# Kernel optimization log

Measured on AMD Instinct MI355X. Metric: run time of the kernel, lower is better.

## Reference

```python
import jax, jax.numpy as jnp
import numpy as np

DEPTH = 5
EPS = 1e-8


def setup_inputs() -> dict:
    key = jax.random.key(0)
    ks = jax.random.split(key, 7)
    N, E, Q = 50000, 1600000, 16
    return {
        "marg_i": jax.random.normal(ks[0], (N, Q), dtype=jnp.float32),
        "cav_ij": jax.random.uniform(ks[1], (E, Q), dtype=jnp.float32),
        "C": jax.random.uniform(ks[2], (Q, Q), dtype=jnp.float32),
        "field_i": jax.random.normal(ks[3], (N, Q), dtype=jnp.float32),
        "edge_dst": jax.random.randint(ks[4], (E,), 0, N, dtype=jnp.int32),
        "a1_src": jax.random.randint(ks[5], (E,), 0, N, dtype=jnp.int32),
        "indice_ij": jax.random.randint(ks[6], (E,), 0, E, dtype=jnp.int32),
    }


def reference(marg_i, cav_ij, C, field_i, edge_dst, a1_src, indice_ij):
    # Belief-propagation layers repeated DEPTH times.
    # B_ @ temp2  -> segment_sum of edge messages into destination nodes [N,Q]
    # A1 @ marg_i -> gather of source-node marginal per edge [E,Q]
    N = field_i.shape[0]

    def step(carry, _):
        marg, cav = carry
        temp2 = jnp.log(cav @ C + EPS)                                  # [E,Q]
        marg = jax.ops.segment_sum(temp2, edge_dst, num_segments=N) + field_i  # [N,Q]
        cav = jax.nn.softmax(marg[a1_src] - temp2[indice_ij], axis=1)  # [E,Q]
        return (marg, cav), None

    (marg, cav), _ = jax.lax.scan(step, (marg_i, cav_ij), None, length=DEPTH)
    return jax.nn.log_softmax(marg, axis=1)
```

## Files before the change

kernel.cpp:

```cpp
#include <hip/hip_runtime.h>
#include <hip/hip_fp16.h>

#define Q 16
#define EPS 1e-8f
#define DEPTH 5

typedef unsigned int u32;
typedef _Float16 h2 __attribute__((ext_vector_type(2)));

__device__ __forceinline__ u32 pack2(float a, float b) {
    __half2 h = __floats2half2_rn(a, b);
    return *(u32*)&h;
}
__device__ __forceinline__ float2 unpack2(u32 u) {
    __half2 h = *(__half2*)&u;
    return __half22float2(h);
}
__device__ __forceinline__ h2 mkh2(float a, float b) {
    h2 v; v[0] = (_Float16)a; v[1] = (_Float16)b; return v;
}


__global__ __launch_bounds__(256) void rank0_kernel(
    const int* __restrict__ dst, int* __restrict__ count,
    int* __restrict__ lr, int E)
{
    int e = blockIdx.x * 256 + threadIdx.x;
    if (e < E) lr[e] = atomicAdd(&count[dst[e]], 1);
}

__global__ __launch_bounds__(256) void scan_partial(
    const int* __restrict__ count, int* __restrict__ partial, int N)
{
    __shared__ int sm[256];
    int i = blockIdx.x * 256 + threadIdx.x;
    sm[threadIdx.x] = (i < N) ? count[i] : 0;
    __syncthreads();
    for (int off = 128; off > 0; off >>= 1) {
        if (threadIdx.x < off) sm[threadIdx.x] += sm[threadIdx.x + off];
        __syncthreads();
    }
    if (threadIdx.x == 0) partial[blockIdx.x] = sm[0];
}

__global__ __launch_bounds__(1024) void scan_top(
    int* __restrict__ partial, int nb)
{
    __shared__ int sm[1024];
    int t = threadIdx.x;
    int v = (t < nb) ? partial[t] : 0;
    sm[t] = v;
    __syncthreads();
    for (int off = 1; off < 1024; off <<= 1) {
        int u = (t >= off) ? sm[t - off] : 0;
        __syncthreads();
        sm[t] += u;
        __syncthreads();
    }
    if (t < nb) partial[t] = sm[t] - v;
}

__global__ __launch_bounds__(256) void scan_final(
    const int* __restrict__ count, const int* __restrict__ partial,
    int* __restrict__ start, int N)
{
    __shared__ int sm[256];
    int i = blockIdx.x * 256 + threadIdx.x;
    int v = (i < N) ? count[i] : 0;
    sm[threadIdx.x] = v;
    __syncthreads();
    for (int off = 1; off < 256; off <<= 1) {
        int u = (threadIdx.x >= off) ? sm[threadIdx.x - off] : 0;
        __syncthreads();
        sm[threadIdx.x] += u;
        __syncthreads();
    }
    int excl = sm[threadIdx.x] - v + partial[blockIdx.x];
    if (i < N) start[i] = excl;
    if (i == N - 1) start[N] = excl + v;
}

__global__ __launch_bounds__(256) void pos_kernel(
    const int* __restrict__ dst, const int* __restrict__ lr,
    const int* __restrict__ start, int* __restrict__ pos, int E)
{
    int e = blockIdx.x * 256 + threadIdx.x;
    if (e < E) pos[e] = start[dst[e]] + lr[e];
}

__global__ __launch_bounds__(256) void scatter_direct(
    const int* __restrict__ a1_src, const int* __restrict__ indice,
    const int* __restrict__ dst, const int* __restrict__ pos,
    int4* __restrict__ sorted, int E)
{
    int e = blockIdx.x * 256 + threadIdx.x;
    if (e < E)
        sorted[pos[e]] = make_int4(a1_src[e], pos[indice[e]], dst[e], e);
}

__global__ __launch_bounds__(256) void meta_pack(
    const int4* __restrict__ sorted, int2* __restrict__ meta2, int E)
{
    int j = blockIdx.x * 256 + threadIdx.x;
    if (j < E) {
        int4 m = sorted[j];
        meta2[j] = make_int2(m.y, (m.z << 16) | m.x);
    }
}

__global__ __launch_bounds__(256) void bnode_build(
    const int* __restrict__ start, int* __restrict__ blist,
    int* __restrict__ bcount, int N)
{
    int n = blockIdx.x * 256 + threadIdx.x;
    if (n >= N) return;
    int slo = start[n], shi = start[n + 1];
    bool need = (slo == shi) || ((slo >> 8) != ((shi - 1) >> 8));
    if (need) {
        int p = atomicAdd(bcount, 1);
        blist[p] = n;
    }
}

__global__ __launch_bounds__(256) void binit(
    const int* __restrict__ blist, const int* __restrict__ bcount,
    const float* __restrict__ field, float* __restrict__ marg)
{
    int idx = blockIdx.x * 256 + threadIdx.x;
    int cnt = *bcount;
    if (idx >= cnt * 4) return;
    int n = blist[idx >> 2], part = idx & 3;
    ((float4*)(marg + (size_t)n * Q))[part] =
        ((const float4*)(field + (size_t)n * Q))[part];
}

template<int MODE>
__global__ __launch_bounds__(256) void fused_round(
    const int4* __restrict__ sorted, const int2* __restrict__ meta2,
    const float* __restrict__ C,
    const float* __restrict__ cav,
    const float* __restrict__ marg_in, const u32* __restrict__ t2_old,
    const int* __restrict__ start, const float* __restrict__ field,
    u32* __restrict__ t2_new, float* __restrict__ marg_out, int E)
{
    __shared__ __align__(16) h2 Csh[Q * 8];
    __shared__ float stage[256 * 17];
    __shared__ int s_nfirst, s_nlast;

    const int tid = threadIdx.x;
    const int blo = blockIdx.x * 256;
    const int bhi = min(blo + 256, E);
    const int j = blo + tid;
    const bool act = (j < E);

    int4 smeta;
    int2 meta;
    float4 m0, m1, m2, m3;
    uint4 r0, r1;
    if (MODE == 0) {
        if (act) {
            smeta = sorted[j];
            const float4* rp = (const float4*)(cav + (size_t)smeta.w * Q);
            m0 = rp[0]; m1 = rp[1]; m2 = rp[2]; m3 = rp[3];
        }
    } else {
        if (act) {
            meta = meta2[j];
            const int src = meta.y & 0xffff;
            const float4* mp = (const float4*)(marg_in + (size_t)src * Q);
            const uint4*  tp = (const uint4*)(t2_old + (size_t)meta.x * 8);
            m0 = mp[0]; m1 = mp[1]; m2 = mp[2]; m3 = mp[3];
            r0 = tp[0]; r1 = tp[1];
        }
    }

    if (tid < 128) {
        int q = tid >> 3, kk = tid & 7;
        Csh[q * 8 + kk] = mkh2(C[(2 * kk) * Q + q], C[(2 * kk + 1) * Q + q]);
    }
    if (act) {
        int mydst = (MODE == 0) ? smeta.z : (int)(((u32)meta.y) >> 16);
        if (j == blo)     s_nfirst = mydst;
        if (j == bhi - 1) s_nlast  = mydst;
    }
    __syncthreads();

    float t[Q];
    if (act) {
        h2 uh[8];
        float s, logs;
        if (MODE == 0) {
            uh[0] = mkh2(m0.x, m0.y); uh[1] = mkh2(m0.z, m0.w);
            uh[2] = mkh2(m1.x, m1.y); uh[3] = mkh2(m1.z, m1.w);
            uh[4] = mkh2(m2.x, m2.y); uh[5] = mkh2(m2.z, m2.w);
            uh[6] = mkh2(m3.x, m3.y); uh[7] = mkh2(m3.z, m3.w);
            s = 1.f; logs = 0.f;
        } else {
            float2 p0 = unpack2(r0.x), p1 = unpack2(r0.y),
                   p2 = unpack2(r0.z), p3 = unpack2(r0.w);
            float2 p4 = unpack2(r1.x), p5 = unpack2(r1.y),
                   p6 = unpack2(r1.z), p7 = unpack2(r1.w);

            float x[Q] = {m0.x - p0.x, m0.y - p0.y, m0.z - p1.x, m0.w - p1.y,
                          m1.x - p2.x, m1.y - p2.y, m1.z - p3.x, m1.w - p3.y,
                          m2.x - p4.x, m2.y - p4.y, m2.z - p5.x, m2.w - p5.y,
                          m3.x - p6.x, m3.y - p6.y, m3.z - p7.x, m3.w - p7.y};

            float mx = x[0];
#pragma unroll
            for (int q = 1; q < Q; ++q) mx = fmaxf(mx, x[q]);
            float u[Q];
            s = 0.f;
#pragma unroll
            for (int q = 0; q < Q; ++q) { u[q] = __expf(x[q] - mx); s += u[q]; }
            logs = __logf(s);
#pragma unroll
            for (int k = 0; k < 8; ++k) uh[k] = mkh2(u[2 * k], u[2 * k + 1]);
        }

        const float base = EPS * s;
#pragma unroll
        for (int q = 0; q < Q; ++q) {
            const uint4* cp = (const uint4*)&Csh[q * 8];
            h2 col[8];
            ((uint4*)col)[0] = cp[0];
            ((uint4*)col)[1] = cp[1];
            float acc = base;
#pragma unroll
            for (int kk = 0; kk < 8; ++kk)
                acc = __builtin_amdgcn_fdot2(uh[kk], col[kk], acc, false);
            t[q] = __logf(acc) - logs;
        }

        if (MODE != 2) {
            uint4 w0, w1;
            w0.x = pack2(t[0],  t[1]);  w0.y = pack2(t[2],  t[3]);
            w0.z = pack2(t[4],  t[5]);  w0.w = pack2(t[6],  t[7]);
            w1.x = pack2(t[8],  t[9]);  w1.y = pack2(t[10], t[11]);
            w1.z = pack2(t[12], t[13]); w1.w = pack2(t[14], t[15]);
            uint4* op = (uint4*)(t2_new + (size_t)j * 8);
            op[0] = w0; op[1] = w1;
        }
    } else {
#pragma unroll
        for (int q = 0; q < Q; ++q) t[q] = 0.f;
    }

#pragma unroll
    for (int q = 0; q < Q; ++q) stage[tid * 17 + q] = t[q];
    __syncthreads();

    const int nfirst = s_nfirst;
    const int ncnt = s_nlast - nfirst + 1;
    for (int k = tid; k < ncnt * Q; k += 256) {
        int ln = k >> 4, q = k & 15;
        int n = nfirst + ln;
        int slo = start[n], shi = start[n + 1];
        int lo = max(slo, blo), hi = min(shi, bhi);
        float s = 0.f;
        for (int sl = lo; sl < hi; ++sl) s += stage[(sl - blo) * 17 + q];
        if (slo >= blo && shi <= bhi)
            marg_out[(size_t)n * Q + q] = s + field[(size_t)n * Q + q];
        else
            atomicAdd(marg_out + (size_t)n * Q + q, s);
    }
}

__global__ __launch_bounds__(256) void node_out(
    const float* __restrict__ marg, float* __restrict__ out, int N)
{
    int i = blockIdx.x * 256 + threadIdx.x;
    if (i >= N) return;

    const float4* mp = (const float4*)(marg + (size_t)i * Q);
    float4 m0 = mp[0], m1 = mp[1], m2 = mp[2], m3 = mp[3];
    float x[Q] = {m0.x, m0.y, m0.z, m0.w, m1.x, m1.y, m1.z, m1.w,
                  m2.x, m2.y, m2.z, m2.w, m3.x, m3.y, m3.z, m3.w};

    float mx = x[0];
#pragma unroll
    for (int q = 1; q < Q; ++q) mx = fmaxf(mx, x[q]);
    float s = 0.f;
#pragma unroll
    for (int q = 0; q < Q; ++q) s += __expf(x[q] - mx);
    float lse = mx + __logf(s);

    float4* op = (float4*)(out + (size_t)i * Q);
    op[0] = make_float4(x[0]  - lse, x[1]  - lse, x[2]  - lse, x[3]  - lse);
    op[1] = make_float4(x[4]  - lse, x[5]  - lse, x[6]  - lse, x[7]  - lse);
    op[2] = make_float4(x[8]  - lse, x[9]  - lse, x[10] - lse, x[11] - lse);
    op[3] = make_float4(x[12] - lse, x[13] - lse, x[14] - lse, x[15] - lse);
}

extern "C" void kernel_launch(void* const* d_in, const int* in_sizes, int n_in,
                              void* d_out, int out_size, void* d_ws, size_t ws_size,
                              hipStream_t stream) {
    const float* cav_in   = (const float*)d_in[1];
    const float* C        = (const float*)d_in[2];
    const float* field_i  = (const float*)d_in[3];
    const int*   edge_dst = (const int*)d_in[4];
    const int*   a1_src   = (const int*)d_in[5];
    const int*   indice   = (const int*)d_in[6];
    float* out = (float*)d_out;

    const int E = in_sizes[4];
    const int N = in_sizes[0] / Q;

    char* ws = (char*)d_ws;
    const size_t t2_bytes   = (size_t)E * 32;
    const size_t i4_bytes   = (size_t)E * 16;
    const size_t node_bytes = (size_t)N * Q * sizeof(float);
    u32*   t2a    = (u32*)ws;                     ws += t2_bytes;
    u32*   t2b    = (u32*)ws;                     ws += t2_bytes;
    int4*  sorted = (int4*)ws;                    ws += i4_bytes;
    int2*  meta2  = (int2*)ws;                    ws += (size_t)E * 8;
    float* marg_a = (float*)ws;                   ws += node_bytes;
    float* marg_b = (float*)ws;                   ws += node_bytes;
    int*   pos    = (int*)ws;                     ws += (size_t)E * 4;
    int*   lr     = (int*)ws;                     ws += (size_t)E * 4;
    int*   count  = (int*)ws;                     ws += (size_t)N * 4;
    int*   bcount = (int*)ws;                     ws += 4;
    int*   start  = (int*)ws;                     ws += (size_t)(N + 1) * 4;
    int*   blist  = (int*)ws;                     ws += (size_t)N * 4;
    int*   partial= (int*)ws;

    const int eb = 256;
    const int eg = (E + eb - 1) / eb;
    const int ng = (N + eb - 1) / eb;

    hipMemsetAsync(count, 0, (size_t)N * 4 + 4, stream);
    rank0_kernel<<<eg, eb, 0, stream>>>(edge_dst, count, lr, E);
    scan_partial<<<ng, eb, 0, stream>>>(count, partial, N);
    scan_top<<<1, 1024, 0, stream>>>(partial, ng);
    scan_final<<<ng, eb, 0, stream>>>(count, partial, start, N);
    pos_kernel<<<eg, eb, 0, stream>>>(edge_dst, lr, start, pos, E);
    scatter_direct<<<eg, eb, 0, stream>>>(a1_src, indice, edge_dst, pos, sorted, E);
    meta_pack<<<eg, eb, 0, stream>>>(sorted, meta2, E);
    bnode_build<<<ng, eb, 0, stream>>>(start, blist, bcount, N);

    u32* t_cur = t2a;
    u32* t_nxt = t2b;
    float* m_in = marg_b;
    float* m_out = marg_a;
    const int bg = (N * 4 + eb - 1) / eb;

    for (int it = 0; it < DEPTH; ++it) {
        binit<<<bg, eb, 0, stream>>>(blist, bcount, field_i, m_out);
        if (it == 0)
            fused_round<0><<<eg, eb, 0, stream>>>(sorted, meta2, C, cav_in,
                                                  nullptr, nullptr, start, field_i,
                                                  t_cur, m_out, E);
        else if (it != DEPTH - 1)
            fused_round<1><<<eg, eb, 0, stream>>>(sorted, meta2, C, nullptr,
                                                  m_in, t_cur, start, field_i,
                                                  t_nxt, m_out, E);
        else
            fused_round<2><<<eg, eb, 0, stream>>>(sorted, meta2, C, nullptr,
                                                  m_in, t_cur, start, field_i,
                                                  nullptr, m_out, E);
        if (it != 0) { u32* tt = t_cur; t_cur = t_nxt; t_nxt = tt; }
        float* tm = m_in; m_in = m_out; m_out = tm;
    }

    node_out<<<ng, eb, 0, stream>>>(m_in, out, N);
}
```

Baseline: 608.0 us.

## Push temp2 to consumer slots via scatter instead of gathering by indice

Builds a CSR of consumers (edges whose indice points at each producer edge) during preprocessing, so each round a producer writes its half-precision temp2 row directly into every consumer's slot. The next round then reads its t2 row contiguously at j instead of gathering at a random sorted index. Metadata is also shrunk from int4/int2 to packed 4-byte arrays. In exchange, preprocessing gains extra atomics, a second multi-level scan and a scatter kernel, and the per-round writes become random scatters whose count varies per edge, which adds divergence.

```diff
diff --git a/kernel.cpp b/kernel.cpp
--- a/kernel.cpp
+++ b/kernel.cpp
@@ -22,19 +22,23 @@
 
 
 __global__ __launch_bounds__(256) void rank0_kernel(
-    const int* __restrict__ dst, int* __restrict__ count,
-    int* __restrict__ lr, int E)
+    const int* __restrict__ dst, const int* __restrict__ indice,
+    int* __restrict__ count, int* __restrict__ ccount,
+    int* __restrict__ lr, int* __restrict__ crank, int E)
 {
     int e = blockIdx.x * 256 + threadIdx.x;
-    if (e < E) lr[e] = atomicAdd(&count[dst[e]], 1);
+    if (e < E) {
+        lr[e]    = atomicAdd(&count[dst[e]], 1);
+        crank[e] = atomicAdd(&ccount[indice[e]], 1);
+    }
 }
 
 __global__ __launch_bounds__(256) void scan_partial(
-    const int* __restrict__ count, int* __restrict__ partial, int N)
+    const int* __restrict__ v, int* __restrict__ partial, int N)
 {
     __shared__ int sm[256];
     int i = blockIdx.x * 256 + threadIdx.x;
-    sm[threadIdx.x] = (i < N) ? count[i] : 0;
+    sm[threadIdx.x] = (i < N) ? v[i] : 0;
     __syncthreads();
     for (int off = 128; off > 0; off >>= 1) {
         if (threadIdx.x < off) sm[threadIdx.x] += sm[threadIdx.x + off];
@@ -61,13 +65,13 @@
 }
 
 __global__ __launch_bounds__(256) void scan_final(
-    const int* __restrict__ count, const int* __restrict__ partial,
-    int* __restrict__ start, int N)
+    const int* __restrict__ v, const int* __restrict__ partial,
+    int* __restrict__ out, int N)
 {
     __shared__ int sm[256];
     int i = blockIdx.x * 256 + threadIdx.x;
-    int v = (i < N) ? count[i] : 0;
-    sm[threadIdx.x] = v;
+    int x = (i < N) ? v[i] : 0;
+    sm[threadIdx.x] = x;
     __syncthreads();
     for (int off = 1; off < 256; off <<= 1) {
         int u = (threadIdx.x >= off) ? sm[threadIdx.x - off] : 0;
@@ -75,36 +79,46 @@
         sm[threadIdx.x] += u;
         __syncthreads();
     }
-    int excl = sm[threadIdx.x] - v + partial[blockIdx.x];
-    if (i < N) start[i] = excl;
-    if (i == N - 1) start[N] = excl + v;
+    int excl = sm[threadIdx.x] - x + partial[blockIdx.x];
+    if (i < N) out[i] = excl;
+    if (i == N - 1) out[N] = excl + x;
 }
 
 __global__ __launch_bounds__(256) void pos_kernel(
     const int* __restrict__ dst, const int* __restrict__ lr,
-    const int* __restrict__ start, int* __restrict__ pos, int E)
+    const int* __restrict__ start, const int* __restrict__ ccount,
+    int* __restrict__ pos, int* __restrict__ slotcc, int E)
 {
     int e = blockIdx.x * 256 + threadIdx.x;
-    if (e < E) pos[e] = start[dst[e]] + lr[e];
+    if (e < E) {
+        int p = start[dst[e]] + lr[e];
+        pos[e] = p;
+        slotcc[p] = ccount[e];
+    }
+}
+
+__global__ __launch_bounds__(256) void cons_scatter(
+    const int* __restrict__ indice, const int* __restrict__ crank,
+    const int* __restrict__ pos, const int* __restrict__ csl,
+    int* __restrict__ cons2, int E)
+{
+    int e = blockIdx.x * 256 + threadIdx.x;
+    if (e < E) {
+        int jp = pos[indice[e]];
+        cons2[csl[jp] + crank[e]] = pos[e];
+    }
 }
 
 __global__ __launch_bounds__(256) void scatter_direct(
-    const int* __restrict__ a1_src, const int* __restrict__ indice,
-    const int* __restrict__ dst, const int* __restrict__ pos,
-    int4* __restrict__ sorted, int E)
+    const int* __restrict__ a1_src, const int* __restrict__ dst,
+    const int* __restrict__ pos,
+    int* __restrict__ meta1, int* __restrict__ m0e, int E)
 {
     int e = blockIdx.x * 256 + threadIdx.x;
-    if (e < E)
-        sorted[pos[e]] = make_int4(a1_src[e], pos[indice[e]], dst[e], e);
-}
-
-__global__ __launch_bounds__(256) void meta_pack(
-    const int4* __restrict__ sorted, int2* __restrict__ meta2, int E)
-{
-    int j = blockIdx.x * 256 + threadIdx.x;
-    if (j < E) {
-        int4 m = sorted[j];
-        meta2[j] = make_int2(m.y, (m.z << 16) | m.x);
+    if (e < E) {
+        int p = pos[e];
+        meta1[p] = (int)(((u32)dst[e] << 16) | (u32)a1_src[e]);
+        m0e[p]   = e;
     }
 }
 
@@ -136,12 +150,13 @@
 
 template<int MODE>
 __global__ __launch_bounds__(256) void fused_round(
-    const int4* __restrict__ sorted, const int2* __restrict__ meta2,
+    const int* __restrict__ meta1, const int* __restrict__ m0e,
+    const int* __restrict__ csl, const int* __restrict__ cons2,
     const float* __restrict__ C,
     const float* __restrict__ cav,
-    const float* __restrict__ marg_in, const u32* __restrict__ t2_old,
+    const float* __restrict__ marg_in, const u32* __restrict__ t2c_cur,
     const int* __restrict__ start, const float* __restrict__ field,
-    u32* __restrict__ t2_new, float* __restrict__ marg_out, int E)
+    u32* __restrict__ t2c_next, float* __restrict__ marg_out, int E)
 {
     __shared__ __align__(16) h2 Csh[Q * 8];
     __shared__ float stage[256 * 17];
@@ -153,22 +168,19 @@
     const int j = blo + tid;
     const bool act = (j < E);
 
-    int4 smeta;
-    int2 meta;
+    int metav = 0, cs0 = 0, cs1 = 0;
     float4 m0, m1, m2, m3;
     uint4 r0, r1;
-    if (MODE == 0) {
-        if (act) {
-            smeta = sorted[j];
-            const float4* rp = (const float4*)(cav + (size_t)smeta.w * Q);
+    if (act) {
+        metav = meta1[j];
+        if (MODE != 2) { cs0 = csl[j]; cs1 = csl[j + 1]; }
+        if (MODE == 0) {
+            const float4* rp = (const float4*)(cav + (size_t)m0e[j] * Q);
             m0 = rp[0]; m1 = rp[1]; m2 = rp[2]; m3 = rp[3];
-        }
-    } else {
-        if (act) {
-            meta = meta2[j];
-            const int src = meta.y & 0xffff;
+        } else {
+            const int src = metav & 0xffff;
             const float4* mp = (const float4*)(marg_in + (size_t)src * Q);
-            const uint4*  tp = (const uint4*)(t2_old + (size_t)meta.x * 8);
+            const uint4*  tp = (const uint4*)(t2c_cur + (size_t)j * 8);
             m0 = mp[0]; m1 = mp[1]; m2 = mp[2]; m3 = mp[3];
             r0 = tp[0]; r1 = tp[1];
         }
@@ -179,7 +191,7 @@
         Csh[q * 8 + kk] = mkh2(C[(2 * kk) * Q + q], C[(2 * kk + 1) * Q + q]);
     }
     if (act) {
-        int mydst = (MODE == 0) ? smeta.z : (int)(((u32)meta.y) >> 16);
+        int mydst = (int)(((u32)metav) >> 16);
         if (j == blo)     s_nfirst = mydst;
         if (j == bhi - 1) s_nlast  = mydst;
     }
@@ -238,8 +250,10 @@
             w0.z = pack2(t[4],  t[5]);  w0.w = pack2(t[6],  t[7]);
             w1.x = pack2(t[8],  t[9]);  w1.y = pack2(t[10], t[11]);
             w1.z = pack2(t[12], t[13]); w1.w = pack2(t[14], t[15]);
-            uint4* op = (uint4*)(t2_new + (size_t)j * 8);
-            op[0] = w0; op[1] = w1;
+            for (int c = cs0; c < cs1; ++c) {
+                uint4* op = (uint4*)(t2c_next + (size_t)cons2[c] * 8);
+                op[0] = w0; op[1] = w1;
+            }
         }
     } else {
 #pragma unroll
@@ -306,56 +320,72 @@
     const int E = in_sizes[4];
     const int N = in_sizes[0] / Q;
 
+    const int eb = 256;
+    const int eg  = (E + eb - 1) / eb;
+    const int ng  = (N + eb - 1) / eb;
+    const int ng2 = (eg + eb - 1) / eb;
+
     char* ws = (char*)d_ws;
     const size_t t2_bytes   = (size_t)E * 32;
-    const size_t i4_bytes   = (size_t)E * 16;
     const size_t node_bytes = (size_t)N * Q * sizeof(float);
-    u32*   t2a    = (u32*)ws;                     ws += t2_bytes;
-    u32*   t2b    = (u32*)ws;                     ws += t2_bytes;
-    int4*  sorted = (int4*)ws;                    ws += i4_bytes;
-    int2*  meta2  = (int2*)ws;                    ws += (size_t)E * 8;
-    float* marg_a = (float*)ws;                   ws += node_bytes;
-    float* marg_b = (float*)ws;                   ws += node_bytes;
-    int*   pos    = (int*)ws;                     ws += (size_t)E * 4;
-    int*   lr     = (int*)ws;                     ws += (size_t)E * 4;
-    int*   count  = (int*)ws;                     ws += (size_t)N * 4;
-    int*   bcount = (int*)ws;                     ws += 4;
-    int*   start  = (int*)ws;                     ws += (size_t)(N + 1) * 4;
-    int*   blist  = (int*)ws;                     ws += (size_t)N * 4;
-    int*   partial= (int*)ws;
-
-    const int eb = 256;
-    const int eg = (E + eb - 1) / eb;
-    const int ng = (N + eb - 1) / eb;
+
+    u32*   t2a    = (u32*)ws;               ws += t2_bytes;
+    u32*   t2b    = (u32*)ws;               ws += t2_bytes;
+    int*   meta1  = (int*)ws;               ws += (size_t)E * 4;
+    int*   csl    = (int*)ws;               ws += (size_t)(E + 1) * 4;
+    int*   ccount = (int*)ws;               ws += (size_t)E * 4;
+    int*   pos    = (int*)ws;               ws += (size_t)E * 4;
+    int*   lr     = (int*)ws;               ws += (size_t)E * 4;
+    int*   crank  = (int*)ws;               ws += (size_t)E * 4;
+    int*   slotcc = (int*)ws;               ws += (size_t)E * 4;
+    float* marg_a = (float*)ws;             ws += node_bytes;
+    float* marg_b = (float*)ws;             ws += node_bytes;
+    int*   count  = (int*)ws;               ws += (size_t)N * 4;
+    int*   bcount = (int*)ws;               ws += 4;
+    int*   start  = (int*)ws;               ws += (size_t)(N + 1) * 4;
+    int*   blist  = (int*)ws;               ws += (size_t)N * 4;
+    int*   partial= (int*)ws;               ws += 1024 * 4;
+    int*   part1  = (int*)ws;               ws += (size_t)eg * 4;
+    int*   part1x = (int*)ws;               ws += (size_t)(eg + 1) * 4;
+    int*   part2  = (int*)ws;
+
+    int* cons2 = ccount;
+    int* m0e   = lr;
 
     hipMemsetAsync(count, 0, (size_t)N * 4 + 4, stream);
-    rank0_kernel<<<eg, eb, 0, stream>>>(edge_dst, count, lr, E);
+    hipMemsetAsync(ccount, 0, (size_t)E * 4, stream);
+    rank0_kernel<<<eg, eb, 0, stream>>>(edge_dst, indice, count, ccount, lr, crank, E);
     scan_partial<<<ng, eb, 0, stream>>>(count, partial, N);
     scan_top<<<1, 1024, 0, stream>>>(partial, ng);
     scan_final<<<ng, eb, 0, stream>>>(count, partial, start, N);
-    pos_kernel<<<eg, eb, 0, stream>>>(edge_dst, lr, start, pos, E);
-    scatter_direct<<<eg, eb, 0, stream>>>(a1_src, indice, edge_dst, pos, sorted, E);
-    meta_pack<<<eg, eb, 0, stream>>>(sorted, meta2, E);
+    pos_kernel<<<eg, eb, 0, stream>>>(edge_dst, lr, start, ccount, pos, slotcc, E);
+    scan_partial<<<eg, eb, 0, stream>>>(slotcc, part1, E);
+    scan_partial<<<ng2, eb, 0, stream>>>(part1, part2, eg);
+    scan_top<<<1, 1024, 0, stream>>>(part2, ng2);
+    scan_final<<<ng2, eb, 0, stream>>>(part1, part2, part1x, eg);
+    scan_final<<<eg, eb, 0, stream>>>(slotcc, part1x, csl, E);
+    cons_scatter<<<eg, eb, 0, stream>>>(indice, crank, pos, csl, cons2, E);
+    scatter_direct<<<eg, eb, 0, stream>>>(a1_src, edge_dst, pos, meta1, m0e, E);
     bnode_build<<<ng, eb, 0, stream>>>(start, blist, bcount, N);
 
     u32* t_cur = t2a;
     u32* t_nxt = t2b;
-    float* m_in = marg_b;
+    float* m_in  = marg_b;
     float* m_out = marg_a;
     const int bg = (N * 4 + eb - 1) / eb;
 
     for (int it = 0; it < DEPTH; ++it) {
         binit<<<bg, eb, 0, stream>>>(blist, bcount, field_i, m_out);
         if (it == 0)
-            fused_round<0><<<eg, eb, 0, stream>>>(sorted, meta2, C, cav_in,
+            fused_round<0><<<eg, eb, 0, stream>>>(meta1, m0e, csl, cons2, C, cav_in,
                                                   nullptr, nullptr, start, field_i,
                                                   t_cur, m_out, E);
         else if (it != DEPTH - 1)
-            fused_round<1><<<eg, eb, 0, stream>>>(sorted, meta2, C, nullptr,
+            fused_round<1><<<eg, eb, 0, stream>>>(meta1, m0e, csl, cons2, C, nullptr,
                                                   m_in, t_cur, start, field_i,
                                                   t_nxt, m_out, E);
         else
-            fused_round<2><<<eg, eb, 0, stream>>>(sorted, meta2, C, nullptr,
+            fused_round<2><<<eg, eb, 0, stream>>>(meta1, m0e, csl, cons2, C, nullptr,
                                                   m_in, t_cur, start, field_i,
                                                   nullptr, m_out, E);
         if (it != 0) { u32* tt = t_cur; t_cur = t_nxt; t_nxt = tt; }
```

After: 817.4 us. +34.4%, slower.

## Drop int4 sorted metadata, write compact meta directly, use 512-thread round blocks

Applied to the files above, without the earlier changes.

The scatter kernel now writes the packed int2 metadata and a separate original-edge index array directly, so the int4 sorted array and the meta_pack pass are gone. The first round reads the int2 metadata plus the edge index instead of an int4. The fused round kernel's block size rises from 256 to 512, with the boundary-node detection shift updated to match. This means fewer partial-node atomics at block boundaries, at the cost of double the shared staging memory per block and possibly lower occupancy.

```diff
diff --git a/kernel.cpp b/kernel.cpp
--- a/kernel.cpp
+++ b/kernel.cpp
@@ -4,6 +4,8 @@
 #define Q 16
 #define EPS 1e-8f
 #define DEPTH 5
+#define BS 512
+#define WSHIFT 9
 
 typedef unsigned int u32;
 typedef _Float16 h2 __attribute__((ext_vector_type(2)));
@@ -91,20 +93,14 @@
 __global__ __launch_bounds__(256) void scatter_direct(
     const int* __restrict__ a1_src, const int* __restrict__ indice,
     const int* __restrict__ dst, const int* __restrict__ pos,
-    int4* __restrict__ sorted, int E)
+    int2* __restrict__ meta2, int* __restrict__ m0e, int E)
 {
     int e = blockIdx.x * 256 + threadIdx.x;
-    if (e < E)
-        sorted[pos[e]] = make_int4(a1_src[e], pos[indice[e]], dst[e], e);
-}
-
-__global__ __launch_bounds__(256) void meta_pack(
-    const int4* __restrict__ sorted, int2* __restrict__ meta2, int E)
-{
-    int j = blockIdx.x * 256 + threadIdx.x;
-    if (j < E) {
-        int4 m = sorted[j];
-        meta2[j] = make_int2(m.y, (m.z << 16) | m.x);
+    if (e < E) {
+        int p = pos[e];
+        meta2[p] = make_int2(pos[indice[e]],
+                             (int)(((u32)dst[e] << 16) | (u32)a1_src[e]));
+        m0e[p] = e;
     }
 }
 
@@ -115,7 +111,7 @@
     int n = blockIdx.x * 256 + threadIdx.x;
     if (n >= N) return;
     int slo = start[n], shi = start[n + 1];
-    bool need = (slo == shi) || ((slo >> 8) != ((shi - 1) >> 8));
+    bool need = (slo == shi) || ((slo >> WSHIFT) != ((shi - 1) >> WSHIFT));
     if (need) {
         int p = atomicAdd(bcount, 1);
         blist[p] = n;
@@ -135,8 +131,8 @@
 }
 
 template<int MODE>
-__global__ __launch_bounds__(256) void fused_round(
-    const int4* __restrict__ sorted, const int2* __restrict__ meta2,
+__global__ __launch_bounds__(BS) void fused_round(
+    const int2* __restrict__ meta2, const int* __restrict__ m0e,
     const float* __restrict__ C,
     const float* __restrict__ cav,
     const float* __restrict__ marg_in, const u32* __restrict__ t2_old,
@@ -144,28 +140,24 @@
     u32* __restrict__ t2_new, float* __restrict__ marg_out, int E)
 {
     __shared__ __align__(16) h2 Csh[Q * 8];
-    __shared__ float stage[256 * 17];
+    __shared__ float stage[BS * 17];
     __shared__ int s_nfirst, s_nlast;
 
     const int tid = threadIdx.x;
-    const int blo = blockIdx.x * 256;
-    const int bhi = min(blo + 256, E);
+    const int blo = blockIdx.x * BS;
+    const int bhi = min(blo + BS, E);
     const int j = blo + tid;
     const bool act = (j < E);
 
-    int4 smeta;
     int2 meta;
     float4 m0, m1, m2, m3;
     uint4 r0, r1;
-    if (MODE == 0) {
-        if (act) {
-            smeta = sorted[j];
-            const float4* rp = (const float4*)(cav + (size_t)smeta.w * Q);
+    if (act) {
+        meta = meta2[j];
+        if (MODE == 0) {
+            const float4* rp = (const float4*)(cav + (size_t)m0e[j] * Q);
             m0 = rp[0]; m1 = rp[1]; m2 = rp[2]; m3 = rp[3];
-        }
-    } else {
-        if (act) {
-            meta = meta2[j];
+        } else {
             const int src = meta.y & 0xffff;
             const float4* mp = (const float4*)(marg_in + (size_t)src * Q);
             const uint4*  tp = (const uint4*)(t2_old + (size_t)meta.x * 8);
@@ -179,7 +171,7 @@
         Csh[q * 8 + kk] = mkh2(C[(2 * kk) * Q + q], C[(2 * kk + 1) * Q + q]);
     }
     if (act) {
-        int mydst = (MODE == 0) ? smeta.z : (int)(((u32)meta.y) >> 16);
+        int mydst = (int)(((u32)meta.y) >> 16);
         if (j == blo)     s_nfirst = mydst;
         if (j == bhi - 1) s_nlast  = mydst;
     }
@@ -252,7 +244,7 @@
 
     const int nfirst = s_nfirst;
     const int ncnt = s_nlast - nfirst + 1;
-    for (int k = tid; k < ncnt * Q; k += 256) {
+    for (int k = tid; k < ncnt * Q; k += BS) {
         int ln = k >> 4, q = k & 15;
         int n = nfirst + ln;
         int slo = start[n], shi = start[n + 1];
@@ -308,12 +300,11 @@
 
     char* ws = (char*)d_ws;
     const size_t t2_bytes   = (size_t)E * 32;
-    const size_t i4_bytes   = (size_t)E * 16;
     const size_t node_bytes = (size_t)N * Q * sizeof(float);
     u32*   t2a    = (u32*)ws;                     ws += t2_bytes;
     u32*   t2b    = (u32*)ws;                     ws += t2_bytes;
-    int4*  sorted = (int4*)ws;                    ws += i4_bytes;
     int2*  meta2  = (int2*)ws;                    ws += (size_t)E * 8;
+    int*   m0e    = (int*)ws;                     ws += (size_t)E * 4;
     float* marg_a = (float*)ws;                   ws += node_bytes;
     float* marg_b = (float*)ws;                   ws += node_bytes;
     int*   pos    = (int*)ws;                     ws += (size_t)E * 4;
@@ -326,6 +317,7 @@
 
     const int eb = 256;
     const int eg = (E + eb - 1) / eb;
+    const int fg = (E + BS - 1) / BS;
     const int ng = (N + eb - 1) / eb;
 
     hipMemsetAsync(count, 0, (size_t)N * 4 + 4, stream);
@@ -334,8 +326,8 @@
     scan_top<<<1, 1024, 0, stream>>>(partial, ng);
     scan_final<<<ng, eb, 0, stream>>>(count, partial, start, N);
     pos_kernel<<<eg, eb, 0, stream>>>(edge_dst, lr, start, pos, E);
-    scatter_direct<<<eg, eb, 0, stream>>>(a1_src, indice, edge_dst, pos, sorted, E);
-    meta_pack<<<eg, eb, 0, stream>>>(sorted, meta2, E);
+    scatter_direct<<<eg, eb, 0, stream>>>(a1_src, indice, edge_dst, pos,
+                                          meta2, m0e, E);
     bnode_build<<<ng, eb, 0, stream>>>(start, blist, bcount, N);
 
     u32* t_cur = t2a;
@@ -347,15 +339,15 @@
     for (int it = 0; it < DEPTH; ++it) {
         binit<<<bg, eb, 0, stream>>>(blist, bcount, field_i, m_out);
         if (it == 0)
-            fused_round<0><<<eg, eb, 0, stream>>>(sorted, meta2, C, cav_in,
+            fused_round<0><<<fg, BS, 0, stream>>>(meta2, m0e, C, cav_in,
                                                   nullptr, nullptr, start, field_i,
                                                   t_cur, m_out, E);
         else if (it != DEPTH - 1)
-            fused_round<1><<<eg, eb, 0, stream>>>(sorted, meta2, C, nullptr,
+            fused_round<1><<<fg, BS, 0, stream>>>(meta2, m0e, C, nullptr,
                                                   m_in, t_cur, start, field_i,
                                                   t_nxt, m_out, E);
         else
-            fused_round<2><<<eg, eb, 0, stream>>>(sorted, meta2, C, nullptr,
+            fused_round<2><<<fg, BS, 0, stream>>>(meta2, m0e, C, nullptr,
                                                   m_in, t_cur, start, field_i,
                                                   nullptr, m_out, E);
         if (it != 0) { u32* tt = t_cur; t_cur = t_nxt; t_nxt = tt; }
```

New measurement: 616.3 us. No clear change (+1.4%).
